# Performance work log

Hardware: AMD Instinct MI355X
Metric: run time of the kernel (lower is better)

Reference implementation:

```python
import jax, jax.numpy as jnp
import numpy as np

E = 512   # embed_size
H = 8     # heads
D = E // H
WIN = 256 # window_size
N = 4     # batch
S = 2048  # seq len (query_len == key_len == value_len)


def setup_inputs() -> dict:
    key = jax.random.key(0)
    ks = jax.random.split(key, 8)
    s = 0.02
    inp = {
        "value": jax.random.normal(ks[0], (N, S, E), jnp.float32),
        "key":   jax.random.normal(ks[1], (N, S, E), jnp.float32),
        "query": jax.random.normal(ks[2], (N, S, E), jnp.float32),
        "mask":  jnp.ones((N, 1, 1, S), jnp.int32),
        # nn.Linear params: y = x @ W.T + b, W shape [out, in]
        "Wv": jax.random.normal(ks[3], (E, E), jnp.float32) * s,
        "bv": jnp.zeros((E,), jnp.float32),
        "Wk": jax.random.normal(ks[4], (E, E), jnp.float32) * s,
        "bk": jnp.zeros((E,), jnp.float32),
        "Wq": jax.random.normal(ks[5], (E, E), jnp.float32) * s,
        "bq": jnp.zeros((E,), jnp.float32),
        "Wo": jax.random.normal(ks[6], (E, E), jnp.float32) * s,
        "bo": jnp.zeros((E,), jnp.float32),
    }
    return inp


def reference(value, key, query, mask, Wv, bv, Wk, bk, Wq, bq, Wo, bo):
    n, q_len, _ = query.shape
    k_len = key.shape[1]
    w = min(WIN, k_len)  # window_size = min(self.window_size, key_len)

    v = (value @ Wv.T + bv).reshape(n, k_len, H, D)
    k = (key   @ Wk.T + bk).reshape(n, k_len, H, D)
    q = (query @ Wq.T + bq).reshape(n, q_len, H, D)

    # Full QK scores; banded window selected below. Position j is inside the
    # window of query i iff  i - w//2 <= j <= i + w//2 (matches the torch
    # per-i slice [max(0,i-w//2), min(k_len, i+w//2+1)) ).
    scores = jnp.einsum('nqhd,nkhd->nhqk', q, k)  # [N,H,Q,K]
    ii = jnp.arange(q_len)[:, None]
    jj = jnp.arange(k_len)[None, :]
    in_win = (jj >= ii - w // 2) & (jj <= ii + w // 2)  # [Q,K]

    # Inside window: scores, masked to -inf where mask == 0.
    # Outside window: entries stay 0 (the torch code zero-inits attention).
    neg_inf = jnp.float32(-jnp.inf)
    banded = jnp.where(mask != 0, scores, neg_inf)          # broadcast [N,1,1,K]
    att_logits = jnp.where(in_win[None, None], banded, 0.0)  # [N,H,Q,K]

    att_logits = att_logits / jnp.sqrt(jnp.float32(E))  # scale by sqrt(embed_size)
    attention = jax.nn.softmax(att_logits, axis=3)

    out = jnp.einsum('nhqk,nkhd->nqhd', attention, v).reshape(n, q_len, E)
    out = out @ Wo.T + bo
    return (out, attention)
```

## Files before the change

### kernel.cpp

```cpp
#include <hip/hip_runtime.h>


typedef unsigned short u16;
typedef __bf16 bf16x8 __attribute__((ext_vector_type(8)));
typedef float  f32x4  __attribute__((ext_vector_type(4)));
typedef u16    u16x8  __attribute__((ext_vector_type(8)));

__device__ __forceinline__ u16 f2bf(float f) {
    union { float f; unsigned u; } x; x.f = f;
    unsigned u = x.u;
    u += 0x7fffu + ((u >> 16) & 1u);
    return (u16)(u >> 16);
}
__device__ __forceinline__ float bf2f(u16 b) {
    union { unsigned u; float f; } x; x.u = ((unsigned)b) << 16;
    return x.f;
}
__device__ __forceinline__ int swzc(int c, int r) {
    return (c < 32) ? (c ^ (r & 7)) : c;
}

struct CvtArgs {
    const float* src[7];
    u16*         dst[7];
};

__global__ __launch_bounds__(256) void cvt_kernel(CvtArgs a) {
    int bid = blockIdx.x;
    int t, blk;
    if (bid < 12288) { t = bid >> 12; blk = bid & 4095; }
    else { int r = bid - 12288; t = 3 + (r >> 8); blk = r & 255; }
    int i = (blk * 256 + threadIdx.x) * 4;
    float4 v = *(const float4*)(a.src[t] + i);
    ushort4 o;
    o.x = f2bf(v.x); o.y = f2bf(v.y); o.z = f2bf(v.z); o.w = f2bf(v.w);
    *(ushort4*)(a.dst[t] + i) = o;
}

template <bool QKV>
__global__ __launch_bounds__(256) void gemm2(
    const u16* __restrict__ A0, const u16* __restrict__ A1, const u16* __restrict__ A2,
    const u16* __restrict__ B,
    const float* __restrict__ b0, const float* __restrict__ b1, const float* __restrict__ b2,
    u16* __restrict__ o0, u16* __restrict__ o1, u16* __restrict__ o2,
    float* __restrict__ fo)
{
    __shared__ __attribute__((aligned(16))) u16 As[128 * 64];
    __shared__ __attribute__((aligned(16))) u16 Bs[128 * 64];

    const int tid  = threadIdx.x;
    const int lane = tid & 63;
    const int w    = tid >> 6;
    const int bm   = blockIdx.x, bn = blockIdx.y;
    const int wm   = w >> 1, wn = w & 1;

    const int t = QKV ? (bn >> 2) : 0;
    const u16* A = (t == 0) ? A0 : (t == 1) ? A1 : A2;
    const u16* Ag = A + (size_t)bm * 128 * 512;
    const u16* Bg = B + (size_t)bn * 128 * 512;

    f32x4 acc[4][4];
#pragma unroll
    for (int m = 0; m < 4; ++m)
#pragma unroll
        for (int n = 0; n < 4; ++n) acc[m][n] = 0;

    const int swc = ((lane & 7) ^ (lane >> 3)) * 8;

    for (int k0 = 0; k0 < 512; k0 += 64) {
#pragma unroll
        for (int i = 0; i < 4; ++i) {
            int row = (i * 4 + w) * 8 + (lane >> 3);
            const u16* ga = Ag + (size_t)row * 512 + k0 + swc;
            const u16* gb = Bg + (size_t)row * 512 + k0 + swc;
            __builtin_amdgcn_global_load_lds(
                (const __attribute__((address_space(1))) void*)ga,
                (__attribute__((address_space(3))) void*)(As + (i * 4 + w) * 512), 16, 0, 0);
            __builtin_amdgcn_global_load_lds(
                (const __attribute__((address_space(1))) void*)gb,
                (__attribute__((address_space(3))) void*)(Bs + (i * 4 + w) * 512), 16, 0, 0);
        }
        __syncthreads();

#pragma unroll
        for (int s = 0; s < 2; ++s) {
            bf16x8 af[4], bf[4];
            int c = s * 4 + (lane >> 4);
#pragma unroll
            for (int m = 0; m < 4; ++m) {
                int r = wm * 64 + m * 16 + (lane & 15);
                af[m] = *(const bf16x8*)(As + r * 64 + ((c ^ (r & 7)) * 8));
                int r2 = wn * 64 + m * 16 + (lane & 15);
                bf[m] = *(const bf16x8*)(Bs + r2 * 64 + ((c ^ (r2 & 7)) * 8));
            }
#pragma unroll
            for (int m = 0; m < 4; ++m)
#pragma unroll
                for (int n = 0; n < 4; ++n)
                    acc[m][n] = __builtin_amdgcn_mfma_f32_16x16x32_bf16(af[m], bf[n], acc[m][n], 0, 0, 0);
        }
        __syncthreads();
    }

    const float* bias = QKV ? ((t == 0) ? b0 : (t == 1) ? b1 : b2) : b0;
    u16* ob = QKV ? ((t == 0) ? o0 : (t == 1) ? o1 : o2) : o0;
    const int clbase = (bn & 3) * 128;

#pragma unroll
    for (int m = 0; m < 4; ++m) {
#pragma unroll
        for (int n = 0; n < 4; ++n) {
            int cl = clbase + wn * 64 + n * 16 + (lane & 15);
            float bb = bias[cl];
#pragma unroll
            for (int reg = 0; reg < 4; ++reg) {
                int row = bm * 128 + wm * 64 + m * 16 + (lane >> 4) * 4 + reg;
                float v = acc[m][n][reg] + bb;
                if (QKV) ob[(size_t)row * 512 + cl] = f2bf(v);
                else     fo[(size_t)row * 512 + cl] = v;
            }
        }
    }
}

__global__ __launch_bounds__(256) void sumv_kernel(const u16* __restrict__ vb,
                                                   float* __restrict__ sumv) {
    __shared__ float part[32][64];
    int nh = blockIdx.x, sb = blockIdx.y;
    int n = nh >> 3, h = nh & 7;
    int tid = threadIdx.x;
    int ch = tid & 7, sg = tid >> 3;
    size_t base = (size_t)n * 2048 * 512 + h * 64;
    float acc[8] = {0, 0, 0, 0, 0, 0, 0, 0};
    for (int p = 0; p < 8; ++p) {
        int s = sb * 256 + p * 32 + sg;
        u16x8 v = *(const u16x8*)(vb + base + (size_t)s * 512 + ch * 8);
#pragma unroll
        for (int r = 0; r < 8; ++r) acc[r] += bf2f(v[r]);
    }
#pragma unroll
    for (int r = 0; r < 8; ++r) part[sg][ch * 8 + r] = acc[r];
    __syncthreads();
    if (tid < 64) {
        float s = 0.f;
#pragma unroll
        for (int g = 0; g < 32; ++g) s += part[g][tid];
        atomicAdd(sumv + nh * 64 + tid, s);
    }
}

__global__ __launch_bounds__(256) void attn_kernel(
    const u16* __restrict__ qb, const u16* __restrict__ kb,
    const u16* __restrict__ vb, const int* __restrict__ mask,
    const float* __restrict__ sumv, float* __restrict__ att,
    u16* __restrict__ oh, float* __restrict__ c_buf) {
    __shared__ __attribute__((aligned(16))) char lds[78848];
    u16*   Qs      = (u16*)lds;
    float* stat_m  = (float*)lds;
    float* stat_rd = (float*)(lds + 128);
    float* stat_c  = (float*)(lds + 256);
    float* red     = (float*)(lds + 384);
    float* red2    = (float*)(lds + 640);
    u16*   Ks      = (u16*)(lds + 4096);
    u16*   Ab      = Ks;
    u16*   Vt      = (u16*)(lds + 4096 + 36864);

    const int tid  = threadIdx.x;
    const int lane = tid & 63;
    const int w    = tid >> 6;
    const int bid  = blockIdx.x;
    const int tile = bid & 63;
    const int h    = (bid >> 6) & 7;
    const int n    = bid >> 9;
    const int i0   = tile * 32;
    const int jlo  = max(0, i0 - 128);
    const float scale = 0.04419417382415922f;

    const size_t base_nh = (size_t)n * 2048 * 512 + h * 64;

    {
        int r = tid >> 3, ch = tid & 7;
        uint4 v = *(const uint4*)(qb + base_nh + (size_t)(i0 + r) * 512 + ch * 8);
        *(uint4*)((char*)Qs + r * 128 + ((ch ^ (r & 7)) << 4)) = v;
    }
    for (int p = 0; p < 9; ++p) {
        int idx = p * 256 + tid;
        int jj = idx >> 3, ch = idx & 7;
        int j = jlo + jj;
        uint4 v = make_uint4(0, 0, 0, 0);
        if (j < 2048) v = *(const uint4*)(kb + base_nh + (size_t)j * 512 + ch * 8);
        *(uint4*)((char*)Ks + jj * 128 + ((ch ^ (jj & 7)) << 4)) = v;
    }
    for (int p = 0; p < 9; ++p) {
        int idx = p * 256 + tid;
        int jj = idx >> 3, ch = idx & 7;
        int j = jlo + jj;
        u16x8 tmp = {0, 0, 0, 0, 0, 0, 0, 0};
        if (j < 2048) tmp = *(const u16x8*)(vb + base_nh + (size_t)j * 512 + ch * 8);
#pragma unroll
        for (int r = 0; r < 8; ++r)
            Vt[(ch * 8 + r) * 296 + jj] = tmp[r];
    }
    __syncthreads();

    const int rbase = (w & 1) * 16;
    const int cbase = (w >> 1) * 144;
    f32x4 acc[9];
#pragma unroll
    for (int f = 0; f < 9; ++f) acc[f] = 0;

    bf16x8 aq[2];
    {
        int r = rbase + (lane & 15);
#pragma unroll
        for (int ks = 0; ks < 2; ++ks) {
            int kc = ks * 4 + (lane >> 4);
            aq[ks] = *(const bf16x8*)((char*)Qs + r * 128 + ((kc ^ (r & 7)) << 4));
        }
    }
#pragma unroll
    for (int f = 0; f < 9; ++f) {
        int jj = cbase + f * 16 + (lane & 15);
#pragma unroll
        for (int ks = 0; ks < 2; ++ks) {
            int kc = ks * 4 + (lane >> 4);
            bf16x8 bk_ = *(const bf16x8*)((char*)Ks + jj * 128 + ((kc ^ (jj & 7)) << 4));
            acc[f] = __builtin_amdgcn_mfma_f32_16x16x32_bf16(aq[ks], bk_, acc[f], 0, 0, 0);
        }
    }
    __syncthreads();

    const int rowg = (lane >> 4) * 4;
    f32x4 lv[9];
    float mx[4] = {-__builtin_inff(), -__builtin_inff(), -__builtin_inff(), -__builtin_inff()};
#pragma unroll
    for (int f = 0; f < 9; ++f) {
        int jj = cbase + f * 16 + (lane & 15);
        int j = jlo + jj;
        int mk = (j < 2048) ? mask[n * 2048 + j] : 0;
#pragma unroll
        for (int reg = 0; reg < 4; ++reg) {
            int i = i0 + rbase + rowg + reg;
            bool inw = (j >= i - 128) && (j <= i + 128) && (j < 2048);
            float val = (inw && mk != 0) ? acc[f][reg] * scale : -__builtin_inff();
            lv[f][reg] = val;
            mx[reg] = fmaxf(mx[reg], val);
        }
    }
#pragma unroll
    for (int mskk = 1; mskk < 16; mskk <<= 1)
#pragma unroll
        for (int reg = 0; reg < 4; ++reg)
            mx[reg] = fmaxf(mx[reg], __shfl_xor(mx[reg], mskk, 64));
    if ((lane & 15) == 0) {
#pragma unroll
        for (int reg = 0; reg < 4; ++reg) red[w * 16 + rowg + reg] = mx[reg];
    }
    __syncthreads();
    if (tid < 32) {
        int r = tid;
        int wa = (r < 16) ? 0 : 1, rr = r & 15;
        stat_m[r] = fmaxf(fmaxf(red[wa * 16 + rr], red[(wa + 2) * 16 + rr]), 0.0f);
    }
    __syncthreads();

    float m4[4];
#pragma unroll
    for (int reg = 0; reg < 4; ++reg) m4[reg] = stat_m[rbase + rowg + reg];
    float sm[4] = {0, 0, 0, 0};
#pragma unroll
    for (int f = 0; f < 9; ++f)
#pragma unroll
        for (int reg = 0; reg < 4; ++reg)
            sm[reg] += __expf(lv[f][reg] - m4[reg]);
#pragma unroll
    for (int mskk = 1; mskk < 16; mskk <<= 1)
#pragma unroll
        for (int reg = 0; reg < 4; ++reg)
            sm[reg] += __shfl_xor(sm[reg], mskk, 64);
    if ((lane & 15) == 0) {
#pragma unroll
        for (int reg = 0; reg < 4; ++reg) red2[w * 16 + rowg + reg] = sm[reg];
    }
    __syncthreads();
    if (tid < 32) {
        int r = tid, gi = i0 + r;
        int wa = (r < 16) ? 0 : 1, rr = r & 15;
        float s = red2[wa * 16 + rr] + red2[(wa + 2) * 16 + rr];
        int lo = max(0, gi - 128), hi = min(2048, gi + 129);
        float em = __expf(-stat_m[r]);
        float denom = s + (float)(2048 - (hi - lo)) * em;
        float rd = 1.0f / denom;
        stat_rd[r] = rd;
        float c = em * rd;
        stat_c[r] = c;
        c_buf[(size_t)(n * 8 + h) * 2048 + gi] = c;
    }
    __syncthreads();

    float rd4[4], c4[4];
#pragma unroll
    for (int reg = 0; reg < 4; ++reg) {
        rd4[reg] = stat_rd[rbase + rowg + reg];
        c4[reg] = stat_c[rbase + rowg + reg];
    }
#pragma unroll
    for (int f = 0; f < 9; ++f) {
        int jj = cbase + f * 16 + (lane & 15);
        int j = jlo + jj;
        int jc = jj >> 3;
#pragma unroll
        for (int reg = 0; reg < 4; ++reg) {
            int it = rbase + rowg + reg;
            int i = i0 + it;
            bool inw = (j >= i - 128) && (j <= i + 128) && (j < 2048);
            float e = __expf(lv[f][reg] - m4[reg]);
            float a = inw ? e * rd4[reg] : c4[reg];
            if (j < 2048)
                att[((size_t)(n * 8 + h) * 2048 + i) * 2048 + j] = a;
            float ab = inw ? (a - c4[reg]) : 0.0f;
            ((u16*)((char*)Ab + it * 576 + (swzc(jc, it) << 4)))[jj & 7] = f2bf(ab);
        }
    }
    __syncthreads();

    const int rb2 = (w & 1) * 16;
    const int db  = (w >> 1) * 32;
    f32x4 po[2];
    po[0] = 0; po[1] = 0;
#pragma unroll
    for (int ks = 0; ks < 9; ++ks) {
        int kc = ks * 4 + (lane >> 4);
        int it = rb2 + (lane & 15);
        bf16x8 af = *(const bf16x8*)((char*)Ab + it * 576 + (swzc(kc, it) << 4));
#pragma unroll
        for (int f = 0; f < 2; ++f) {
            int d = db + f * 16 + (lane & 15);
            bf16x8 bv_ = *(const bf16x8*)(Vt + d * 296 + kc * 8);
            po[f] = __builtin_amdgcn_mfma_f32_16x16x32_bf16(af, bv_, po[f], 0, 0, 0);
        }
    }
    {
        const float* svp = sumv + (size_t)(n * 8 + h) * 64;
#pragma unroll
        for (int f = 0; f < 2; ++f) {
            int d = db + f * 16 + (lane & 15);
            float sv = svp[d];
#pragma unroll
            for (int reg = 0; reg < 4; ++reg) {
                int it = rb2 + rowg + reg;
                float val = po[f][reg] + stat_c[it] * sv;
                oh[base_nh + (size_t)(i0 + it) * 512 + d] = f2bf(val);
            }
        }
    }
}

__global__ __launch_bounds__(256) void fill_kernel(const float* __restrict__ c_buf,
                                                   float* __restrict__ att) {
    __shared__ float cs[32];
    int bid = blockIdx.x;
    int tile = bid & 63, h = (bid >> 6) & 7, n = bid >> 9;
    int i0 = tile * 32;
    int jlo = max(0, i0 - 128);
    int jend = min(2048, jlo + 288);
    int j4lo = jlo >> 2, j4end = jend >> 2;
    int tid = threadIdx.x;
    if (tid < 32) cs[tid] = c_buf[(size_t)(n * 8 + h) * 2048 + i0 + tid];
    __syncthreads();
    size_t rowbase = ((size_t)(n * 8 + h) * 2048 + i0) * 2048;
    for (int idx = tid; idx < 32 * 512; idx += 256) {
        int r = idx >> 9, j4 = idx & 511;
        if (j4 >= j4lo && j4 < j4end) continue;
        float c = cs[r];
        *(float4*)(att + rowbase + (size_t)r * 2048 + j4 * 4) = make_float4(c, c, c, c);
    }
}

extern "C" void kernel_launch(void* const* d_in, const int* in_sizes, int n_in,
                              void* d_out, int out_size, void* d_ws, size_t ws_size,
                              hipStream_t stream) {
    const float* value = (const float*)d_in[0];
    const float* key_  = (const float*)d_in[1];
    const float* query = (const float*)d_in[2];
    const int*   mask  = (const int*)d_in[3];
    const float* Wv = (const float*)d_in[4];
    const float* bv = (const float*)d_in[5];
    const float* Wk = (const float*)d_in[6];
    const float* bk = (const float*)d_in[7];
    const float* Wq = (const float*)d_in[8];
    const float* bq = (const float*)d_in[9];
    const float* Wo = (const float*)d_in[10];
    const float* bo = (const float*)d_in[11];

    char* ws = (char*)d_ws;
    size_t off = 0;
    auto carve = [&](size_t bytes) -> char* {
        char* p = ws + off;
        off += (bytes + 255) & ~(size_t)255;
        return p;
    };
    const size_t XB = (size_t)8192 * 512 * 2;
    const size_t WB = (size_t)512 * 512 * 2;
    u16* xqb  = (u16*)carve(XB);
    u16* xkb  = (u16*)carve(XB);
    u16* xvb  = (u16*)carve(XB);
    u16* wqkv = (u16*)carve(3 * WB);
    u16* wob  = (u16*)carve(WB);
    u16* qb   = (u16*)carve(XB);
    u16* kb   = (u16*)carve(XB);
    u16* vb2  = (u16*)carve(XB);
    u16* ohb  = (u16*)carve(XB);
    float* sumv  = (float*)carve(2048 * sizeof(float));
    float* c_buf = (float*)carve((size_t)65536 * sizeof(float));

    hipMemsetAsync(sumv, 0, 2048 * sizeof(float), stream);

    CvtArgs ca;
    ca.src[0] = query; ca.dst[0] = xqb;
    ca.src[1] = key_;  ca.dst[1] = xkb;
    ca.src[2] = value; ca.dst[2] = xvb;
    ca.src[3] = Wq;    ca.dst[3] = wqkv;
    ca.src[4] = Wk;    ca.dst[4] = wqkv + (size_t)512 * 512;
    ca.src[5] = Wv;    ca.dst[5] = wqkv + (size_t)1024 * 512;
    ca.src[6] = Wo;    ca.dst[6] = wob;

    cvt_kernel<<<dim3(13312), 256, 0, stream>>>(ca);
    gemm2<true><<<dim3(64, 12), 256, 0, stream>>>(
        xqb, xkb, xvb, wqkv, bq, bk, bv, qb, kb, vb2, nullptr);
    sumv_kernel<<<dim3(32, 8), 256, 0, stream>>>(vb2, sumv);

    float* att = (float*)d_out + (size_t)4 * 2048 * 512;
    attn_kernel<<<dim3(2048), 256, 0, stream>>>(qb, kb, vb2, mask, sumv, att, ohb, c_buf);
    gemm2<false><<<dim3(64, 4), 256, 0, stream>>>(
        ohb, nullptr, nullptr, wob, bo, nullptr, nullptr, nullptr, nullptr, nullptr, (float*)d_out);
    fill_kernel<<<dim3(2048), 256, 0, stream>>>(c_buf, att);
}
```

Measured before the change: 697.9 us.

## Fuse V column sums into QKV GEMM, retile output GEMM, async LDS loads in attention

Removes the separate sumv kernel by reducing the V projection accumulators in the QKV GEMM epilogue with shuffles and atomics. Note this sums fp32 values before bf16 rounding. Adds a dedicated output-projection GEMM with 128x64 tiles, giving twice as many blocks. In the attention kernel, Q and K tiles load through global_load_lds, block IDs are remapped, and the transposed V layout is XOR-swizzled to cut LDS bank conflicts. The main total is probably dominated by the large attention-matrix fill, so gains are modest.

```diff
diff --git a/kernel.cpp b/kernel.cpp
--- a/kernel.cpp
+++ b/kernel.cpp
@@ -5,16 +5,17 @@
 typedef __bf16 bf16x8 __attribute__((ext_vector_type(8)));
 typedef float  f32x4  __attribute__((ext_vector_type(4)));
 typedef u16    u16x8  __attribute__((ext_vector_type(8)));
+
+#define GLOAD_LDS(gsrc, ldst)                                                  \
+    __builtin_amdgcn_global_load_lds(                                          \
+        (const __attribute__((address_space(1))) void*)(gsrc),                 \
+        (__attribute__((address_space(3))) void*)(ldst), 16, 0, 0)
 
 __device__ __forceinline__ u16 f2bf(float f) {
     union { float f; unsigned u; } x; x.f = f;
     unsigned u = x.u;
     u += 0x7fffu + ((u >> 16) & 1u);
     return (u16)(u >> 16);
-}
-__device__ __forceinline__ float bf2f(u16 b) {
-    union { unsigned u; float f; } x; x.u = ((unsigned)b) << 16;
-    return x.f;
 }
 __device__ __forceinline__ int swzc(int c, int r) {
     return (c < 32) ? (c ^ (r & 7)) : c;
@@ -37,13 +38,12 @@
     *(ushort4*)(a.dst[t] + i) = o;
 }
 
-template <bool QKV>
-__global__ __launch_bounds__(256) void gemm2(
+__global__ __launch_bounds__(256) void gemm_qkv(
     const u16* __restrict__ A0, const u16* __restrict__ A1, const u16* __restrict__ A2,
     const u16* __restrict__ B,
     const float* __restrict__ b0, const float* __restrict__ b1, const float* __restrict__ b2,
     u16* __restrict__ o0, u16* __restrict__ o1, u16* __restrict__ o2,
-    float* __restrict__ fo)
+    float* __restrict__ sumv)
 {
     __shared__ __attribute__((aligned(16))) u16 As[128 * 64];
     __shared__ __attribute__((aligned(16))) u16 Bs[128 * 64];
@@ -54,7 +54,7 @@
     const int bm   = blockIdx.x, bn = blockIdx.y;
     const int wm   = w >> 1, wn = w & 1;
 
-    const int t = QKV ? (bn >> 2) : 0;
+    const int t = bn >> 2;
     const u16* A = (t == 0) ? A0 : (t == 1) ? A1 : A2;
     const u16* Ag = A + (size_t)bm * 128 * 512;
     const u16* Bg = B + (size_t)bn * 128 * 512;
@@ -70,15 +70,10 @@
     for (int k0 = 0; k0 < 512; k0 += 64) {
 #pragma unroll
         for (int i = 0; i < 4; ++i) {
-            int row = (i * 4 + w) * 8 + (lane >> 3);
-            const u16* ga = Ag + (size_t)row * 512 + k0 + swc;
-            const u16* gb = Bg + (size_t)row * 512 + k0 + swc;
-            __builtin_amdgcn_global_load_lds(
-                (const __attribute__((address_space(1))) void*)ga,
-                (__attribute__((address_space(3))) void*)(As + (i * 4 + w) * 512), 16, 0, 0);
-            __builtin_amdgcn_global_load_lds(
-                (const __attribute__((address_space(1))) void*)gb,
-                (__attribute__((address_space(3))) void*)(Bs + (i * 4 + w) * 512), 16, 0, 0);
+            int g = i * 4 + w;
+            int row = g * 8 + (lane >> 3);
+            GLOAD_LDS(Ag + (size_t)row * 512 + k0 + swc, As + g * 512);
+            GLOAD_LDS(Bg + (size_t)row * 512 + k0 + swc, Bs + g * 512);
         }
         __syncthreads();
 
@@ -102,8 +97,8 @@
         __syncthreads();
     }
 
-    const float* bias = QKV ? ((t == 0) ? b0 : (t == 1) ? b1 : b2) : b0;
-    u16* ob = QKV ? ((t == 0) ? o0 : (t == 1) ? o1 : o2) : o0;
+    const float* bias = (t == 0) ? b0 : (t == 1) ? b1 : b2;
+    u16* ob = (t == 0) ? o0 : (t == 1) ? o1 : o2;
     const int clbase = (bn & 3) * 128;
 
 #pragma unroll
@@ -115,37 +110,100 @@
 #pragma unroll
             for (int reg = 0; reg < 4; ++reg) {
                 int row = bm * 128 + wm * 64 + m * 16 + (lane >> 4) * 4 + reg;
-                float v = acc[m][n][reg] + bb;
-                if (QKV) ob[(size_t)row * 512 + cl] = f2bf(v);
-                else     fo[(size_t)row * 512 + cl] = v;
-            }
-        }
-    }
-}
-
-__global__ __launch_bounds__(256) void sumv_kernel(const u16* __restrict__ vb,
-                                                   float* __restrict__ sumv) {
-    __shared__ float part[32][64];
-    int nh = blockIdx.x, sb = blockIdx.y;
-    int n = nh >> 3, h = nh & 7;
-    int tid = threadIdx.x;
-    int ch = tid & 7, sg = tid >> 3;
-    size_t base = (size_t)n * 2048 * 512 + h * 64;
-    float acc[8] = {0, 0, 0, 0, 0, 0, 0, 0};
-    for (int p = 0; p < 8; ++p) {
-        int s = sb * 256 + p * 32 + sg;
-        u16x8 v = *(const u16x8*)(vb + base + (size_t)s * 512 + ch * 8);
-#pragma unroll
-        for (int r = 0; r < 8; ++r) acc[r] += bf2f(v[r]);
-    }
-#pragma unroll
-    for (int r = 0; r < 8; ++r) part[sg][ch * 8 + r] = acc[r];
-    __syncthreads();
-    if (tid < 64) {
-        float s = 0.f;
-#pragma unroll
-        for (int g = 0; g < 32; ++g) s += part[g][tid];
-        atomicAdd(sumv + nh * 64 + tid, s);
+                ob[(size_t)row * 512 + cl] = f2bf(acc[m][n][reg] + bb);
+            }
+        }
+    }
+
+    if (t == 2) {
+        int nb = bm >> 4;
+#pragma unroll
+        for (int n = 0; n < 4; ++n) {
+            float s = 0.f;
+#pragma unroll
+            for (int m = 0; m < 4; ++m)
+#pragma unroll
+                for (int reg = 0; reg < 4; ++reg) s += acc[m][n][reg];
+            s += __shfl_xor(s, 16, 64);
+            s += __shfl_xor(s, 32, 64);
+            if (lane < 16) {
+                int cl = clbase + wn * 64 + n * 16 + lane;
+                atomicAdd(sumv + nb * 512 + cl, s);
+            }
+        }
+    }
+}
+
+__global__ __launch_bounds__(256) void gemm_o(
+    const u16* __restrict__ A, const u16* __restrict__ B,
+    const float* __restrict__ bias, float* __restrict__ fo)
+{
+    __shared__ __attribute__((aligned(16))) u16 As[128 * 64];
+    __shared__ __attribute__((aligned(16))) u16 Bs[64 * 64];
+
+    const int tid  = threadIdx.x;
+    const int lane = tid & 63;
+    const int w    = tid >> 6;
+    const int bm   = blockIdx.x, bn = blockIdx.y;
+    const int wm   = w >> 1, wn = w & 1;
+
+    const u16* Ag = A + (size_t)bm * 128 * 512;
+    const u16* Bg = B + (size_t)bn * 64 * 512;
+
+    f32x4 acc[4][2];
+#pragma unroll
+    for (int m = 0; m < 4; ++m) { acc[m][0] = 0; acc[m][1] = 0; }
+
+    const int swc = ((lane & 7) ^ (lane >> 3)) * 8;
+
+    for (int k0 = 0; k0 < 512; k0 += 64) {
+#pragma unroll
+        for (int i = 0; i < 4; ++i) {
+            int g = i * 4 + w;
+            GLOAD_LDS(Ag + (size_t)(g * 8 + (lane >> 3)) * 512 + k0 + swc, As + g * 512);
+        }
+#pragma unroll
+        for (int i = 0; i < 2; ++i) {
+            int g = i * 4 + w;
+            GLOAD_LDS(Bg + (size_t)(g * 8 + (lane >> 3)) * 512 + k0 + swc, Bs + g * 512);
+        }
+        __syncthreads();
+
+#pragma unroll
+        for (int s = 0; s < 2; ++s) {
+            bf16x8 af[4], bf[2];
+            int c = s * 4 + (lane >> 4);
+#pragma unroll
+            for (int m = 0; m < 4; ++m) {
+                int r = wm * 64 + m * 16 + (lane & 15);
+                af[m] = *(const bf16x8*)(As + r * 64 + ((c ^ (r & 7)) * 8));
+            }
+#pragma unroll
+            for (int n = 0; n < 2; ++n) {
+                int r2 = wn * 32 + n * 16 + (lane & 15);
+                bf[n] = *(const bf16x8*)(Bs + r2 * 64 + ((c ^ (r2 & 7)) * 8));
+            }
+#pragma unroll
+            for (int m = 0; m < 4; ++m)
+#pragma unroll
+                for (int n = 0; n < 2; ++n)
+                    acc[m][n] = __builtin_amdgcn_mfma_f32_16x16x32_bf16(af[m], bf[n], acc[m][n], 0, 0, 0);
+        }
+        __syncthreads();
+    }
+
+#pragma unroll
+    for (int m = 0; m < 4; ++m) {
+#pragma unroll
+        for (int n = 0; n < 2; ++n) {
+            int cl = bn * 64 + wn * 32 + n * 16 + (lane & 15);
+            float bb = bias[cl];
+#pragma unroll
+            for (int reg = 0; reg < 4; ++reg) {
+                int row = bm * 128 + wm * 64 + m * 16 + (lane >> 4) * 4 + reg;
+                fo[(size_t)row * 512 + cl] = acc[m][n][reg] + bb;
+            }
+        }
     }
 }
 
@@ -168,7 +226,8 @@
     const int tid  = threadIdx.x;
     const int lane = tid & 63;
     const int w    = tid >> 6;
-    const int bid  = blockIdx.x;
+    const int bid0 = blockIdx.x;
+    const int bid  = (bid0 & 7) * 256 + (bid0 >> 3);
     const int tile = bid & 63;
     const int h    = (bid >> 6) & 7;
     const int n    = bid >> 9;
@@ -177,19 +236,14 @@
     const float scale = 0.04419417382415922f;
 
     const size_t base_nh = (size_t)n * 2048 * 512 + h * 64;
-
-    {
-        int r = tid >> 3, ch = tid & 7;
-        uint4 v = *(const uint4*)(qb + base_nh + (size_t)(i0 + r) * 512 + ch * 8);
-        *(uint4*)((char*)Qs + r * 128 + ((ch ^ (r & 7)) << 4)) = v;
-    }
+    const int lr = lane >> 3;
+    const int swg = ((lane & 7) ^ lr) * 8;
+
+    GLOAD_LDS(qb + base_nh + (size_t)(i0 + w * 8 + lr) * 512 + swg, Qs + w * 512);
     for (int p = 0; p < 9; ++p) {
-        int idx = p * 256 + tid;
-        int jj = idx >> 3, ch = idx & 7;
-        int j = jlo + jj;
-        uint4 v = make_uint4(0, 0, 0, 0);
-        if (j < 2048) v = *(const uint4*)(kb + base_nh + (size_t)j * 512 + ch * 8);
-        *(uint4*)((char*)Ks + jj * 128 + ((ch ^ (jj & 7)) << 4)) = v;
+        int g = p * 4 + w;
+        int j = min(jlo + g * 8 + lr, 2047);
+        GLOAD_LDS(kb + base_nh + (size_t)j * 512 + swg, Ks + g * 512);
     }
     for (int p = 0; p < 9; ++p) {
         int idx = p * 256 + tid;
@@ -197,9 +251,11 @@
         int j = jlo + jj;
         u16x8 tmp = {0, 0, 0, 0, 0, 0, 0, 0};
         if (j < 2048) tmp = *(const u16x8*)(vb + base_nh + (size_t)j * 512 + ch * 8);
+        int jc = jj >> 3, jr = jj & 7;
+        int pjc = (jc < 32) ? (jc ^ ch) : jc;
 #pragma unroll
         for (int r = 0; r < 8; ++r)
-            Vt[(ch * 8 + r) * 296 + jj] = tmp[r];
+            Vt[(ch * 8 + r) * 296 + pjc * 8 + jr] = tmp[r];
     }
     __syncthreads();
 
@@ -215,7 +271,7 @@
 #pragma unroll
         for (int ks = 0; ks < 2; ++ks) {
             int kc = ks * 4 + (lane >> 4);
-            aq[ks] = *(const bf16x8*)((char*)Qs + r * 128 + ((kc ^ (r & 7)) << 4));
+            aq[ks] = *(const bf16x8*)(Qs + r * 64 + ((kc ^ (r & 7)) * 8));
         }
     }
 #pragma unroll
@@ -224,7 +280,7 @@
 #pragma unroll
         for (int ks = 0; ks < 2; ++ks) {
             int kc = ks * 4 + (lane >> 4);
-            bf16x8 bk_ = *(const bf16x8*)((char*)Ks + jj * 128 + ((kc ^ (jj & 7)) << 4));
+            bf16x8 bk_ = *(const bf16x8*)(Ks + jj * 64 + ((kc ^ (jj & 7)) * 8));
             acc[f] = __builtin_amdgcn_mfma_f32_16x16x32_bf16(aq[ks], bk_, acc[f], 0, 0, 0);
         }
     }
@@ -336,12 +392,13 @@
 #pragma unroll
         for (int f = 0; f < 2; ++f) {
             int d = db + f * 16 + (lane & 15);
-            bf16x8 bv_ = *(const bf16x8*)(Vt + d * 296 + kc * 8);
+            int phys = (kc < 32) ? (kc ^ (d >> 3)) : kc;
+            bf16x8 bv_ = *(const bf16x8*)(Vt + d * 296 + phys * 8);
             po[f] = __builtin_amdgcn_mfma_f32_16x16x32_bf16(af, bv_, po[f], 0, 0, 0);
         }
     }
     {
-        const float* svp = sumv + (size_t)(n * 8 + h) * 64;
+        const float* svp = sumv + (size_t)n * 512 + h * 64;
 #pragma unroll
         for (int f = 0; f < 2; ++f) {
             int d = db + f * 16 + (lane & 15);
@@ -426,13 +483,11 @@
     ca.src[6] = Wo;    ca.dst[6] = wob;
 
     cvt_kernel<<<dim3(13312), 256, 0, stream>>>(ca);
-    gemm2<true><<<dim3(64, 12), 256, 0, stream>>>(
-        xqb, xkb, xvb, wqkv, bq, bk, bv, qb, kb, vb2, nullptr);
-    sumv_kernel<<<dim3(32, 8), 256, 0, stream>>>(vb2, sumv);
+    gemm_qkv<<<dim3(64, 12), 256, 0, stream>>>(
+        xqb, xkb, xvb, wqkv, bq, bk, bv, qb, kb, vb2, sumv);
 
     float* att = (float*)d_out + (size_t)4 * 2048 * 512;
     attn_kernel<<<dim3(2048), 256, 0, stream>>>(qb, kb, vb2, mask, sumv, att, ohb, c_buf);
-    gemm2<false><<<dim3(64, 4), 256, 0, stream>>>(
-        ohb, nullptr, nullptr, wob, bo, nullptr, nullptr, nullptr, nullptr, nullptr, (float*)d_out);
+    gemm_o<<<dim3(64, 8), 256, 0, stream>>>(ohb, wob, bo, (float*)d_out);
     fill_kernel<<<dim3(2048), 256, 0, stream>>>(c_buf, att);
 }
```

Result: faster. 670.9 us (-3.9%).
